# Optimization experiments

Hardware: AMD Instinct MI355X
Metric: run time of the kernel (lower is better)

## Reference

```python
import jax, jax.numpy as jnp
import numpy as np

N_NODES = 100000
N_EDGES = 1600000
IN_FEATS = 64
NUM_CLASSES = 64


def setup_inputs() -> dict:
    key = jax.random.key(0)
    k1, k2, k3, k4, k5, k6 = jax.random.split(key, 6)
    in_feat = jax.random.normal(k1, (N_NODES, IN_FEATS), dtype=jnp.float32)
    src = jax.random.randint(k2, (N_EDGES,), 0, N_NODES, dtype=jnp.int32)
    dst = jax.random.randint(k3, (N_EDGES,), 0, N_NODES, dtype=jnp.int32)
    scale = 1.0 / np.sqrt(IN_FEATS)
    W_self = jax.random.normal(k4, (IN_FEATS, NUM_CLASSES), dtype=jnp.float32) * scale
    W_neigh = jax.random.normal(k5, (IN_FEATS, NUM_CLASSES), dtype=jnp.float32) * scale
    bias = jax.random.normal(k6, (NUM_CLASSES,), dtype=jnp.float32) * 0.01
    return {"in_feat": in_feat, "src": src, "dst": dst,
            "W_self": W_self, "W_neigh": W_neigh, "bias": bias}


def reference(in_feat, src, dst, W_self, W_neigh, bias):
    # SAGEConv with 'mean' aggregator (DGL semantics):
    #   h_neigh[v] = mean over incoming edges (u->v) of in_feat[u]; 0 if no in-edges
    #   out = fc_self(x) + fc_neigh(h_neigh) + bias, then sigmoid
    n = in_feat.shape[0]
    msg = in_feat[src]                                            # [E, F] gather
    agg = jax.ops.segment_sum(msg, dst, num_segments=n)           # [N, F]
    deg = jax.ops.segment_sum(jnp.ones((src.shape[0],), jnp.float32), dst,
                              num_segments=n)                     # [N]
    h_neigh = agg / jnp.maximum(deg, 1.0)[:, None]                # mean, 0 for isolated
    out = in_feat @ W_self + h_neigh @ W_neigh + bias
    return jax.nn.sigmoid(out)
```

## Files before the change

### kernel.cpp

```cpp
#include <hip/hip_runtime.h>


constexpr int NN = 100000;
constexpr int NE = 1600000;
constexpr int F  = 64;
constexpr int RB = 256;
constexpr int NB = (NN + RB - 1) / RB;
constexpr int CH = 8192;
constexpr int PB = (NE + CH - 1) / CH;
constexpr int PREPB = (NN * F / 8 + 1024 + 255) / 256;
constexpr int SCAP = 3072;
constexpr int NP = 12;

typedef short bf16x8 __attribute__((ext_vector_type(8)));
typedef float f32x4  __attribute__((ext_vector_type(4)));
typedef float f32x2  __attribute__((ext_vector_type(2)));
typedef unsigned short u16;
typedef u16 u16x8 __attribute__((ext_vector_type(8)));

__device__ __forceinline__ u16 f2bf(float f) {
    unsigned u = __float_as_uint(f);
    unsigned r = (u + 0x7FFF + ((u >> 16) & 1)) >> 16;
    return (u16)r;
}

__device__ __forceinline__ void acc8pk(f32x2& a0, f32x2& a1, f32x2& a2, f32x2& a3,
                                       int2 qq) {
#if __has_builtin(__builtin_amdgcn_cvt_pk_f32_fp8)
    a0 += __builtin_amdgcn_cvt_pk_f32_fp8(qq.x, false);
    a1 += __builtin_amdgcn_cvt_pk_f32_fp8(qq.x, true);
    a2 += __builtin_amdgcn_cvt_pk_f32_fp8(qq.y, false);
    a3 += __builtin_amdgcn_cvt_pk_f32_fp8(qq.y, true);
#else
    a0[0] += __builtin_amdgcn_cvt_f32_fp8(qq.x, 0);
    a0[1] += __builtin_amdgcn_cvt_f32_fp8(qq.x, 1);
    a1[0] += __builtin_amdgcn_cvt_f32_fp8(qq.x, 2);
    a1[1] += __builtin_amdgcn_cvt_f32_fp8(qq.x, 3);
    a2[0] += __builtin_amdgcn_cvt_f32_fp8(qq.y, 0);
    a2[1] += __builtin_amdgcn_cvt_f32_fp8(qq.y, 1);
    a3[0] += __builtin_amdgcn_cvt_f32_fp8(qq.y, 2);
    a3[1] += __builtin_amdgcn_cvt_f32_fp8(qq.y, 3);
#endif
}

__global__ __launch_bounds__(256) void k_prep_hist(
    const float* __restrict__ x, const float* __restrict__ Ws,
    const float* __restrict__ Wn, const int* __restrict__ dst,
    unsigned char* __restrict__ x8, u16* __restrict__ xb, u16* __restrict__ Bt,
    int* __restrict__ gcount, int* __restrict__ donecnt,
    int* __restrict__ basep, int* __restrict__ cursor)
{
    const int bid = blockIdx.x;
    const int t   = threadIdx.x;

    if (bid < PREPB) {
        const int i = bid * 256 + t;
        if (i < NN * F / 8) {
            const int o = i * 8;
            float4 a = *(const float4*)&x[o];
            float4 b = *(const float4*)&x[o + 4];
            int lo = 0, hi = 0;
            lo = __builtin_amdgcn_cvt_pk_fp8_f32(a.x, a.y, lo, false);
            lo = __builtin_amdgcn_cvt_pk_fp8_f32(a.z, a.w, lo, true);
            hi = __builtin_amdgcn_cvt_pk_fp8_f32(b.x, b.y, hi, false);
            hi = __builtin_amdgcn_cvt_pk_fp8_f32(b.z, b.w, hi, true);
            *(int2*)&x8[o] = make_int2(lo, hi);
            u16x8 r;
            r[0] = f2bf(a.x); r[1] = f2bf(a.y); r[2] = f2bf(a.z); r[3] = f2bf(a.w);
            r[4] = f2bf(b.x); r[5] = f2bf(b.y); r[6] = f2bf(b.z); r[7] = f2bf(b.w);
            *(u16x8*)&xb[o] = r;
        } else if (i < NN * F / 8 + 1024) {
            const int j  = i - NN * F / 8;
            const int n  = j >> 4;
            const int kb = (j & 15) * 8;
            u16x8 r;
#pragma unroll
            for (int jj = 0; jj < 8; ++jj) {
                const int kk = kb + jj;
                const float w = (kk < 64) ? Ws[kk * 64 + n] : Wn[(kk - 64) * 64 + n];
                r[jj] = f2bf(w);
            }
            *(u16x8*)&Bt[n * 128 + kb] = r;
        }
        return;
    }

    __shared__ int h[NB];
    __shared__ int lastflag;
    for (int i = t; i < NB; i += 256) h[i] = 0;
    __syncthreads();
    const int hb  = bid - PREPB;
    const int b0  = hb * CH;
    const int end = min(b0 + CH, NE);
    for (int i = b0 + t * 4; i < end; i += 1024) {
        int4 d = *(const int4*)&dst[i];
        atomicAdd(&h[d.x >> 8], 1);
        atomicAdd(&h[d.y >> 8], 1);
        atomicAdd(&h[d.z >> 8], 1);
        atomicAdd(&h[d.w >> 8], 1);
    }
    __syncthreads();
    for (int i = t; i < NB; i += 256)
        if (h[i]) atomicAdd(&gcount[i], h[i]);

    __threadfence();
    if (t == 0) lastflag = (atomicAdd(donecnt, 1) == PB - 1);
    __syncthreads();
    if (!lastflag || t >= 64) return;

    int v[7], pre[7], s = 0;
#pragma unroll
    for (int j = 0; j < 7; ++j) {
        const int idx = t * 7 + j;
        v[j] = (idx < NB) ? atomicAdd(&gcount[idx], 0) : 0;
        pre[j] = s;
        s += v[j];
    }
    int run = s;
#pragma unroll
    for (int o = 1; o < 64; o <<= 1) {
        const int n = __shfl_up(run, o);
        if (t >= o) run += n;
    }
    const int lbase = run - s;
#pragma unroll
    for (int j = 0; j < 7; ++j) {
        const int idx = t * 7 + j;
        if (idx < NB) {
            basep[idx]  = lbase + pre[j];
            cursor[idx] = lbase + pre[j];
        }
    }
}

__global__ __launch_bounds__(512) void k_part(const int* __restrict__ src,
                                              const int* __restrict__ dst,
                                              int* __restrict__ cursor,
                                              unsigned* __restrict__ packed) {
    __shared__ unsigned stage[CH];
    __shared__ unsigned short bkt[CH];
    __shared__ int hist[NB], lscan[NB], lcur[NB], gpos[NB];
    __shared__ int tmp[512];

    const int t   = threadIdx.x;
    const int b0  = blockIdx.x * CH;
    const int cnt = min(CH, NE - b0);

    for (int i = t; i < NB; i += 512) hist[i] = 0;
    __syncthreads();

    int4 sv[4], dv[4];
#pragma unroll
    for (int j = 0; j < 4; ++j) {
        const int idx = j * 2048 + t * 4;
        if (idx < cnt) {
            sv[j] = *(const int4*)&src[b0 + idx];
            dv[j] = *(const int4*)&dst[b0 + idx];
            atomicAdd(&hist[dv[j].x >> 8], 1);
            atomicAdd(&hist[dv[j].y >> 8], 1);
            atomicAdd(&hist[dv[j].z >> 8], 1);
            atomicAdd(&hist[dv[j].w >> 8], 1);
        }
    }
    __syncthreads();

    int val = (t < NB) ? hist[t] : 0;
    tmp[t] = val;
    __syncthreads();
    int s = val;
    for (int o = 1; o < 512; o <<= 1) {
        int add = (t >= o) ? tmp[t - o] : 0;
        __syncthreads();
        s += add;
        tmp[t] = s;
        __syncthreads();
    }
    if (t < NB) {
        lscan[t] = s - val;
        lcur[t]  = s - val;
        gpos[t]  = val ? atomicAdd(&cursor[t], val) : 0;
    }
    __syncthreads();

#pragma unroll
    for (int j = 0; j < 4; ++j) {
        const int idx = j * 2048 + t * 4;
        if (idx < cnt) {
            const int ss[4] = {sv[j].x, sv[j].y, sv[j].z, sv[j].w};
            const int dd[4] = {dv[j].x, dv[j].y, dv[j].z, dv[j].w};
#pragma unroll
            for (int q = 0; q < 4; ++q) {
                const int b = dd[q] >> 8;
                const int p = atomicAdd(&lcur[b], 1);
                stage[p] = ((unsigned)(dd[q] & 255) << 17) | (unsigned)ss[q];
                bkt[p]   = (unsigned short)b;
            }
        }
    }
    __syncthreads();

    for (int i = t; i < cnt; i += 512) {
        const int b = bkt[i];
        packed[gpos[b] + (i - lscan[b])] = stage[i];
    }
}

__global__ __launch_bounds__(512) void k_fused(
    const unsigned char* __restrict__ x8, const u16* __restrict__ xb,
    const unsigned* __restrict__ packed, const int* __restrict__ basep,
    const u16* __restrict__ Bt, const float* __restrict__ bias,
    float* __restrict__ out)
{
    __shared__ u16 At[64 * 128];
    __shared__ unsigned stage[SCAP];
    __shared__ int hist[128], cur[128], exar[128];

    const int blk  = blockIdx.x;
    const int bu   = blk >> 1;
    const int hh   = blk & 1;
    const int base = bu * RB + hh * 128;
    const int t    = threadIdx.x;

    const int e0 = basep[bu];
    const int e1 = (bu == NB - 1) ? NE : basep[bu + 1];
    const int m  = e1 - e0;

    if (t < 128) hist[t] = 0;
    __syncthreads();

    unsigned pv[NP];
#pragma unroll
    for (int j = 0; j < NP; ++j) {
        const int i = t + j * 512;
        unsigned p = 0xFFFFFFFFu;
        if (i < m) p = packed[e0 + i];
        pv[j] = p;
        if (p != 0xFFFFFFFFu && ((p >> 24) & 1u) == (unsigned)hh)
            atomicAdd(&hist[(p >> 17) & 127], 1);
    }
    __syncthreads();

    if (t < 64) {
        const int v0 = hist[2 * t], v1 = hist[2 * t + 1];
        const int sv = v0 + v1;
        int run = sv;
#pragma unroll
        for (int o = 1; o < 64; o <<= 1) {
            const int n = __shfl_up(run, o);
            if (t >= o) run += n;
        }
        const int b0 = run - sv;
        exar[2 * t] = b0;      exar[2 * t + 1] = b0 + v0;
        cur[2 * t]  = b0;      cur[2 * t + 1]  = b0 + v0;
    }
    __syncthreads();

#pragma unroll
    for (int j = 0; j < NP; ++j) {
        const unsigned p = pv[j];
        if (p != 0xFFFFFFFFu && ((p >> 24) & 1u) == (unsigned)hh) {
            const int pos = atomicAdd(&cur[(p >> 17) & 127], 1);
            if (pos < SCAP) stage[pos] = p & 0x1FFFFu;
        }
    }
    __syncthreads();

    const int r    = t >> 3;
    const int cg   = t & 7;
    const int w    = t >> 6;
    const int lane = t & 63;
    const int tr   = w >> 1;
    const int nh   = w & 1;
    const int r16  = lane & 15;
    const int kg   = lane >> 4;

    for (int q = 0; q < 2; ++q) {
        const int nb64 = base + q * 64;
        const int nv_r = min(64, NN - nb64);

        if (nv_r > 0 && r < nv_r) {
            const int ln = q * 64 + r;
            const int dg = hist[ln];
            const int s0 = exar[ln];
            f32x2 a0 = {0.f, 0.f}, a1 = a0, a2 = a0, a3 = a0;
            int e = 0;
            for (; e + 4 <= dg; e += 4) {
                const int i0 = stage[s0 + e + 0];
                const int i1 = stage[s0 + e + 1];
                const int i2 = stage[s0 + e + 2];
                const int i3 = stage[s0 + e + 3];
                int2 q0 = *(const int2*)&x8[(size_t)i0 * F + cg * 8];
                int2 q1 = *(const int2*)&x8[(size_t)i1 * F + cg * 8];
                int2 q2 = *(const int2*)&x8[(size_t)i2 * F + cg * 8];
                int2 q3 = *(const int2*)&x8[(size_t)i3 * F + cg * 8];
                acc8pk(a0, a1, a2, a3, q0);
                acc8pk(a0, a1, a2, a3, q1);
                acc8pk(a0, a1, a2, a3, q2);
                acc8pk(a0, a1, a2, a3, q3);
            }
            for (; e < dg; ++e) {
                int2 qv = *(const int2*)&x8[(size_t)stage[s0 + e] * F + cg * 8];
                acc8pk(a0, a1, a2, a3, qv);
            }
            const float inv = 1.0f / fmaxf((float)dg, 1.0f);
            u16x8 hbv;
            hbv[0] = f2bf(a0[0] * inv); hbv[1] = f2bf(a0[1] * inv);
            hbv[2] = f2bf(a1[0] * inv); hbv[3] = f2bf(a1[1] * inv);
            hbv[4] = f2bf(a2[0] * inv); hbv[5] = f2bf(a2[1] * inv);
            hbv[6] = f2bf(a3[0] * inv); hbv[7] = f2bf(a3[1] * inv);
            const int bh = (8 + cg) ^ (r & 15);
            *(u16x8*)&At[r * 128 + bh * 8] = hbv;
            const int bx = cg ^ (r & 15);
            *(u16x8*)&At[r * 128 + bx * 8] = *(const u16x8*)&xb[(size_t)(nb64 + r) * F + cg * 8];
        }
        __syncthreads();

        if (nv_r > 0 && tr * 16 < nv_r) {
            bf16x8 bfr[4][2];
#pragma unroll
            for (int t4 = 0; t4 < 4; ++t4)
#pragma unroll
                for (int uu = 0; uu < 2; ++uu) {
                    const int n = (nh * 2 + uu) * 16 + r16;
                    bfr[t4][uu] = *(const bf16x8*)&Bt[n * 128 + t4 * 32 + kg * 8];
                }
            const float b0 = bias[(nh * 2 + 0) * 16 + r16];
            const float b1 = bias[(nh * 2 + 1) * 16 + r16];

            const int row = tr * 16 + r16;
            bf16x8 a[4];
#pragma unroll
            for (int t4 = 0; t4 < 4; ++t4) {
                const int blk16 = (t4 * 4 + kg) ^ (row & 15);
                a[t4] = *(const bf16x8*)&At[row * 128 + blk16 * 8];
            }

            f32x4 c0 = {0.f, 0.f, 0.f, 0.f}, c1 = c0;
            c0 = __builtin_amdgcn_mfma_f32_16x16x32_bf16(a[0], bfr[0][0], c0, 0, 0, 0);
            c0 = __builtin_amdgcn_mfma_f32_16x16x32_bf16(a[1], bfr[1][0], c0, 0, 0, 0);
            c0 = __builtin_amdgcn_mfma_f32_16x16x32_bf16(a[2], bfr[2][0], c0, 0, 0, 0);
            c0 = __builtin_amdgcn_mfma_f32_16x16x32_bf16(a[3], bfr[3][0], c0, 0, 0, 0);
            c1 = __builtin_amdgcn_mfma_f32_16x16x32_bf16(a[0], bfr[0][1], c1, 0, 0, 0);
            c1 = __builtin_amdgcn_mfma_f32_16x16x32_bf16(a[1], bfr[1][1], c1, 0, 0, 0);
            c1 = __builtin_amdgcn_mfma_f32_16x16x32_bf16(a[2], bfr[2][1], c1, 0, 0, 0);
            c1 = __builtin_amdgcn_mfma_f32_16x16x32_bf16(a[3], bfr[3][1], c1, 0, 0, 0);

            float* orow = out + (size_t)(nb64 + tr * 16) * 64;
#pragma unroll
            for (int rr = 0; rr < 4; ++rr) {
                const int ro = (kg * 4 + rr) * 64;
                orow[ro + (nh * 2 + 0) * 16 + r16] = 1.0f / (1.0f + __expf(-(c0[rr] + b0)));
                orow[ro + (nh * 2 + 1) * 16 + r16] = 1.0f / (1.0f + __expf(-(c1[rr] + b1)));
            }
        }
        __syncthreads();
    }
}

extern "C" void kernel_launch(void* const* d_in, const int* in_sizes, int n_in,
                              void* d_out, int out_size, void* d_ws, size_t ws_size,
                              hipStream_t stream) {
    const float* x    = (const float*)d_in[0];
    const int*   src  = (const int*)d_in[1];
    const int*   dst  = (const int*)d_in[2];
    const float* Ws   = (const float*)d_in[3];
    const float* Wn   = (const float*)d_in[4];
    const float* bias = (const float*)d_in[5];
    float* out = (float*)d_out;

    int* gcount  = (int*)d_ws;
    int* donecnt = gcount + NB;
    int* basep   = donecnt + 1;
    int* cursor  = basep + NB;
    unsigned* packed = (unsigned*)(cursor + NB);
    unsigned char* x8 = (unsigned char*)(packed + NE);
    u16* xb = (u16*)(x8 + (size_t)NN * F);
    u16* Bt = xb + (size_t)NN * F;

    hipMemsetAsync(gcount, 0, (size_t)(NB + 1) * sizeof(int), stream);

    k_prep_hist<<<PREPB + PB, 256, 0, stream>>>(x, Ws, Wn, dst, x8, xb, Bt,
                                                gcount, donecnt, basep, cursor);
    k_part <<<PB, 512, 0, stream>>>(src, dst, cursor, packed);
    k_fused<<<(NN + 127) / 128, 512, 0, stream>>>(x8, xb, packed, basep, Bt, bias, out);
}
```

Measured before the change: 102.8 us.

## Split fused SAGE blocks into quarters, drop bf16 x copy, sort edges by source half

The fused aggregation/GEMM kernel now runs four 64-node blocks per 256-node bucket instead of two 128-node blocks. Each block handles a single GEMM tile, with an overflow loop for edges beyond the register-held portion. The bf16 copy of x written in the prep kernel is removed, and the fused kernel converts fp32 x to bf16 on the fly. This trades a 12.8 MB write for a larger fp32 read. Edges are also keyed by a src-half bit so each node's neighbor list is grouped by source half for gather locality, and the partition chunk shrinks to 2048 so each thread handles one int4.

```diff
diff --git a/kernel.cpp b/kernel.cpp
--- a/kernel.cpp
+++ b/kernel.cpp
@@ -6,11 +6,12 @@
 constexpr int F  = 64;
 constexpr int RB = 256;
 constexpr int NB = (NN + RB - 1) / RB;
-constexpr int CH = 8192;
+constexpr int CH = 2048;
 constexpr int PB = (NE + CH - 1) / CH;
 constexpr int PREPB = (NN * F / 8 + 1024 + 255) / 256;
-constexpr int SCAP = 3072;
-constexpr int NP = 12;
+constexpr int HALF = 50000;
+constexpr int NP  = 9;
+constexpr int SCAP = 2048;
 
 typedef short bf16x8 __attribute__((ext_vector_type(8)));
 typedef float f32x4  __attribute__((ext_vector_type(4)));
@@ -46,7 +47,7 @@
 __global__ __launch_bounds__(256) void k_prep_hist(
     const float* __restrict__ x, const float* __restrict__ Ws,
     const float* __restrict__ Wn, const int* __restrict__ dst,
-    unsigned char* __restrict__ x8, u16* __restrict__ xb, u16* __restrict__ Bt,
+    unsigned char* __restrict__ x8, u16* __restrict__ Bt,
     int* __restrict__ gcount, int* __restrict__ donecnt,
     int* __restrict__ basep, int* __restrict__ cursor)
 {
@@ -65,10 +66,6 @@
             hi = __builtin_amdgcn_cvt_pk_fp8_f32(b.x, b.y, hi, false);
             hi = __builtin_amdgcn_cvt_pk_fp8_f32(b.z, b.w, hi, true);
             *(int2*)&x8[o] = make_int2(lo, hi);
-            u16x8 r;
-            r[0] = f2bf(a.x); r[1] = f2bf(a.y); r[2] = f2bf(a.z); r[3] = f2bf(a.w);
-            r[4] = f2bf(b.x); r[5] = f2bf(b.y); r[6] = f2bf(b.z); r[7] = f2bf(b.w);
-            *(u16x8*)&xb[o] = r;
         } else if (i < NN * F / 8 + 1024) {
             const int j  = i - NN * F / 8;
             const int n  = j >> 4;
@@ -149,18 +146,16 @@
     for (int i = t; i < NB; i += 512) hist[i] = 0;
     __syncthreads();
 
-    int4 sv[4], dv[4];
-#pragma unroll
-    for (int j = 0; j < 4; ++j) {
-        const int idx = j * 2048 + t * 4;
-        if (idx < cnt) {
-            sv[j] = *(const int4*)&src[b0 + idx];
-            dv[j] = *(const int4*)&dst[b0 + idx];
-            atomicAdd(&hist[dv[j].x >> 8], 1);
-            atomicAdd(&hist[dv[j].y >> 8], 1);
-            atomicAdd(&hist[dv[j].z >> 8], 1);
-            atomicAdd(&hist[dv[j].w >> 8], 1);
-        }
+    int4 sv, dv;
+    const int idx = t * 4;
+    const bool act = idx < cnt;
+    if (act) {
+        sv = *(const int4*)&src[b0 + idx];
+        dv = *(const int4*)&dst[b0 + idx];
+        atomicAdd(&hist[dv.x >> 8], 1);
+        atomicAdd(&hist[dv.y >> 8], 1);
+        atomicAdd(&hist[dv.z >> 8], 1);
+        atomicAdd(&hist[dv.w >> 8], 1);
     }
     __syncthreads();
 
@@ -182,19 +177,16 @@
     }
     __syncthreads();
 
-#pragma unroll
-    for (int j = 0; j < 4; ++j) {
-        const int idx = j * 2048 + t * 4;
-        if (idx < cnt) {
-            const int ss[4] = {sv[j].x, sv[j].y, sv[j].z, sv[j].w};
-            const int dd[4] = {dv[j].x, dv[j].y, dv[j].z, dv[j].w};
-#pragma unroll
-            for (int q = 0; q < 4; ++q) {
-                const int b = dd[q] >> 8;
-                const int p = atomicAdd(&lcur[b], 1);
-                stage[p] = ((unsigned)(dd[q] & 255) << 17) | (unsigned)ss[q];
-                bkt[p]   = (unsigned short)b;
-            }
+    if (act) {
+        const int ss[4] = {sv.x, sv.y, sv.z, sv.w};
+        const int dd[4] = {dv.x, dv.y, dv.z, dv.w};
+#pragma unroll
+        for (int q = 0; q < 4; ++q) {
+            const int b = dd[q] >> 8;
+            const int p = atomicAdd(&lcur[b], 1);
+            stage[p] = ((unsigned)(dd[q] & 255) << 18) |
+                       ((unsigned)(ss[q] >= HALF) << 17) | (unsigned)ss[q];
+            bkt[p]   = (unsigned short)b;
         }
     }
     __syncthreads();
@@ -206,7 +198,7 @@
 }
 
 __global__ __launch_bounds__(512) void k_fused(
-    const unsigned char* __restrict__ x8, const u16* __restrict__ xb,
+    const unsigned char* __restrict__ x8, const float* __restrict__ x,
     const unsigned* __restrict__ packed, const int* __restrict__ basep,
     const u16* __restrict__ Bt, const float* __restrict__ bias,
     float* __restrict__ out)
@@ -216,10 +208,11 @@
     __shared__ int hist[128], cur[128], exar[128];
 
     const int blk  = blockIdx.x;
-    const int bu   = blk >> 1;
-    const int hh   = blk & 1;
-    const int base = bu * RB + hh * 128;
+    const int bu   = blk >> 2;
+    const int qq   = blk & 3;
+    const int base = bu * RB + qq * 64;
     const int t    = threadIdx.x;
+    const int nv   = min(64, NN - base);
 
     const int e0 = basep[bu];
     const int e1 = (bu == NB - 1) ? NE : basep[bu + 1];
@@ -235,8 +228,12 @@
         unsigned p = 0xFFFFFFFFu;
         if (i < m) p = packed[e0 + i];
         pv[j] = p;
-        if (p != 0xFFFFFFFFu && ((p >> 24) & 1u) == (unsigned)hh)
+        if (p != 0xFFFFFFFFu && (int)((p >> 24) & 3) == qq)
             atomicAdd(&hist[(p >> 17) & 127], 1);
+    }
+    for (int i = NP * 512 + t; i < m; i += 512) {
+        const unsigned p = packed[e0 + i];
+        if ((int)((p >> 24) & 3) == qq) atomicAdd(&hist[(p >> 17) & 127], 1);
     }
     __syncthreads();
 
@@ -258,102 +255,107 @@
 #pragma unroll
     for (int j = 0; j < NP; ++j) {
         const unsigned p = pv[j];
-        if (p != 0xFFFFFFFFu && ((p >> 24) & 1u) == (unsigned)hh) {
+        if (p != 0xFFFFFFFFu && (int)((p >> 24) & 3) == qq) {
             const int pos = atomicAdd(&cur[(p >> 17) & 127], 1);
             if (pos < SCAP) stage[pos] = p & 0x1FFFFu;
         }
     }
-    __syncthreads();
-
-    const int r    = t >> 3;
-    const int cg   = t & 7;
+    for (int i = NP * 512 + t; i < m; i += 512) {
+        const unsigned p = packed[e0 + i];
+        if ((int)((p >> 24) & 3) == qq) {
+            const int pos = atomicAdd(&cur[(p >> 17) & 127], 1);
+            if (pos < SCAP) stage[pos] = p & 0x1FFFFu;
+        }
+    }
+    __syncthreads();
+
+    const int r  = t >> 3;
+    const int cg = t & 7;
+    if (r < nv) {
+        const int dg = hist[2 * r] + hist[2 * r + 1];
+        const int s0 = exar[2 * r];
+        f32x2 a0 = {0.f, 0.f}, a1 = a0, a2 = a0, a3 = a0;
+        int e = 0;
+        for (; e + 4 <= dg; e += 4) {
+            const int i0 = stage[s0 + e + 0];
+            const int i1 = stage[s0 + e + 1];
+            const int i2 = stage[s0 + e + 2];
+            const int i3 = stage[s0 + e + 3];
+            int2 q0 = *(const int2*)&x8[(size_t)i0 * F + cg * 8];
+            int2 q1 = *(const int2*)&x8[(size_t)i1 * F + cg * 8];
+            int2 q2 = *(const int2*)&x8[(size_t)i2 * F + cg * 8];
+            int2 q3 = *(const int2*)&x8[(size_t)i3 * F + cg * 8];
+            acc8pk(a0, a1, a2, a3, q0);
+            acc8pk(a0, a1, a2, a3, q1);
+            acc8pk(a0, a1, a2, a3, q2);
+            acc8pk(a0, a1, a2, a3, q3);
+        }
+        for (; e < dg; ++e) {
+            int2 qv = *(const int2*)&x8[(size_t)stage[s0 + e] * F + cg * 8];
+            acc8pk(a0, a1, a2, a3, qv);
+        }
+        const float inv = 1.0f / fmaxf((float)dg, 1.0f);
+        u16x8 hbv;
+        hbv[0] = f2bf(a0[0] * inv); hbv[1] = f2bf(a0[1] * inv);
+        hbv[2] = f2bf(a1[0] * inv); hbv[3] = f2bf(a1[1] * inv);
+        hbv[4] = f2bf(a2[0] * inv); hbv[5] = f2bf(a2[1] * inv);
+        hbv[6] = f2bf(a3[0] * inv); hbv[7] = f2bf(a3[1] * inv);
+        const int bh = (8 + cg) ^ (r & 15);
+        *(u16x8*)&At[r * 128 + bh * 8] = hbv;
+
+        float4 xa = *(const float4*)&x[(size_t)(base + r) * F + cg * 8];
+        float4 xc = *(const float4*)&x[(size_t)(base + r) * F + cg * 8 + 4];
+        u16x8 xv;
+        xv[0] = f2bf(xa.x); xv[1] = f2bf(xa.y); xv[2] = f2bf(xa.z); xv[3] = f2bf(xa.w);
+        xv[4] = f2bf(xc.x); xv[5] = f2bf(xc.y); xv[6] = f2bf(xc.z); xv[7] = f2bf(xc.w);
+        const int bx = cg ^ (r & 15);
+        *(u16x8*)&At[r * 128 + bx * 8] = xv;
+    }
+    __syncthreads();
+
     const int w    = t >> 6;
     const int lane = t & 63;
     const int tr   = w >> 1;
-    const int nh   = w & 1;
-    const int r16  = lane & 15;
-    const int kg   = lane >> 4;
-
-    for (int q = 0; q < 2; ++q) {
-        const int nb64 = base + q * 64;
-        const int nv_r = min(64, NN - nb64);
-
-        if (nv_r > 0 && r < nv_r) {
-            const int ln = q * 64 + r;
-            const int dg = hist[ln];
-            const int s0 = exar[ln];
-            f32x2 a0 = {0.f, 0.f}, a1 = a0, a2 = a0, a3 = a0;
-            int e = 0;
-            for (; e + 4 <= dg; e += 4) {
-                const int i0 = stage[s0 + e + 0];
-                const int i1 = stage[s0 + e + 1];
-                const int i2 = stage[s0 + e + 2];
-                const int i3 = stage[s0 + e + 3];
-                int2 q0 = *(const int2*)&x8[(size_t)i0 * F + cg * 8];
-                int2 q1 = *(const int2*)&x8[(size_t)i1 * F + cg * 8];
-                int2 q2 = *(const int2*)&x8[(size_t)i2 * F + cg * 8];
-                int2 q3 = *(const int2*)&x8[(size_t)i3 * F + cg * 8];
-                acc8pk(a0, a1, a2, a3, q0);
-                acc8pk(a0, a1, a2, a3, q1);
-                acc8pk(a0, a1, a2, a3, q2);
-                acc8pk(a0, a1, a2, a3, q3);
-            }
-            for (; e < dg; ++e) {
-                int2 qv = *(const int2*)&x8[(size_t)stage[s0 + e] * F + cg * 8];
-                acc8pk(a0, a1, a2, a3, qv);
-            }
-            const float inv = 1.0f / fmaxf((float)dg, 1.0f);
-            u16x8 hbv;
-            hbv[0] = f2bf(a0[0] * inv); hbv[1] = f2bf(a0[1] * inv);
-            hbv[2] = f2bf(a1[0] * inv); hbv[3] = f2bf(a1[1] * inv);
-            hbv[4] = f2bf(a2[0] * inv); hbv[5] = f2bf(a2[1] * inv);
-            hbv[6] = f2bf(a3[0] * inv); hbv[7] = f2bf(a3[1] * inv);
-            const int bh = (8 + cg) ^ (r & 15);
-            *(u16x8*)&At[r * 128 + bh * 8] = hbv;
-            const int bx = cg ^ (r & 15);
-            *(u16x8*)&At[r * 128 + bx * 8] = *(const u16x8*)&xb[(size_t)(nb64 + r) * F + cg * 8];
-        }
-        __syncthreads();
-
-        if (nv_r > 0 && tr * 16 < nv_r) {
-            bf16x8 bfr[4][2];
-#pragma unroll
-            for (int t4 = 0; t4 < 4; ++t4)
-#pragma unroll
-                for (int uu = 0; uu < 2; ++uu) {
-                    const int n = (nh * 2 + uu) * 16 + r16;
-                    bfr[t4][uu] = *(const bf16x8*)&Bt[n * 128 + t4 * 32 + kg * 8];
-                }
-            const float b0 = bias[(nh * 2 + 0) * 16 + r16];
-            const float b1 = bias[(nh * 2 + 1) * 16 + r16];
-
-            const int row = tr * 16 + r16;
-            bf16x8 a[4];
-#pragma unroll
-            for (int t4 = 0; t4 < 4; ++t4) {
-                const int blk16 = (t4 * 4 + kg) ^ (row & 15);
-                a[t4] = *(const bf16x8*)&At[row * 128 + blk16 * 8];
-            }
-
-            f32x4 c0 = {0.f, 0.f, 0.f, 0.f}, c1 = c0;
-            c0 = __builtin_amdgcn_mfma_f32_16x16x32_bf16(a[0], bfr[0][0], c0, 0, 0, 0);
-            c0 = __builtin_amdgcn_mfma_f32_16x16x32_bf16(a[1], bfr[1][0], c0, 0, 0, 0);
-            c0 = __builtin_amdgcn_mfma_f32_16x16x32_bf16(a[2], bfr[2][0], c0, 0, 0, 0);
-            c0 = __builtin_amdgcn_mfma_f32_16x16x32_bf16(a[3], bfr[3][0], c0, 0, 0, 0);
-            c1 = __builtin_amdgcn_mfma_f32_16x16x32_bf16(a[0], bfr[0][1], c1, 0, 0, 0);
-            c1 = __builtin_amdgcn_mfma_f32_16x16x32_bf16(a[1], bfr[1][1], c1, 0, 0, 0);
-            c1 = __builtin_amdgcn_mfma_f32_16x16x32_bf16(a[2], bfr[2][1], c1, 0, 0, 0);
-            c1 = __builtin_amdgcn_mfma_f32_16x16x32_bf16(a[3], bfr[3][1], c1, 0, 0, 0);
-
-            float* orow = out + (size_t)(nb64 + tr * 16) * 64;
-#pragma unroll
-            for (int rr = 0; rr < 4; ++rr) {
-                const int ro = (kg * 4 + rr) * 64;
-                orow[ro + (nh * 2 + 0) * 16 + r16] = 1.0f / (1.0f + __expf(-(c0[rr] + b0)));
-                orow[ro + (nh * 2 + 1) * 16 + r16] = 1.0f / (1.0f + __expf(-(c1[rr] + b1)));
-            }
-        }
-        __syncthreads();
+    if (tr * 16 >= nv) return;
+    const int nh  = w & 1;
+    const int r16 = lane & 15;
+    const int kg  = lane >> 4;
+
+    bf16x8 bfr[4][2];
+#pragma unroll
+    for (int t4 = 0; t4 < 4; ++t4)
+#pragma unroll
+        for (int uu = 0; uu < 2; ++uu) {
+            const int n = (nh * 2 + uu) * 16 + r16;
+            bfr[t4][uu] = *(const bf16x8*)&Bt[n * 128 + t4 * 32 + kg * 8];
+        }
+    const float b0 = bias[(nh * 2 + 0) * 16 + r16];
+    const float b1 = bias[(nh * 2 + 1) * 16 + r16];
+
+    const int row = tr * 16 + r16;
+    bf16x8 a[4];
+#pragma unroll
+    for (int t4 = 0; t4 < 4; ++t4) {
+        const int blk16 = (t4 * 4 + kg) ^ (row & 15);
+        a[t4] = *(const bf16x8*)&At[row * 128 + blk16 * 8];
+    }
+
+    f32x4 c0 = {0.f, 0.f, 0.f, 0.f}, c1 = c0;
+    c0 = __builtin_amdgcn_mfma_f32_16x16x32_bf16(a[0], bfr[0][0], c0, 0, 0, 0);
+    c0 = __builtin_amdgcn_mfma_f32_16x16x32_bf16(a[1], bfr[1][0], c0, 0, 0, 0);
+    c0 = __builtin_amdgcn_mfma_f32_16x16x32_bf16(a[2], bfr[2][0], c0, 0, 0, 0);
+    c0 = __builtin_amdgcn_mfma_f32_16x16x32_bf16(a[3], bfr[3][0], c0, 0, 0, 0);
+    c1 = __builtin_amdgcn_mfma_f32_16x16x32_bf16(a[0], bfr[0][1], c1, 0, 0, 0);
+    c1 = __builtin_amdgcn_mfma_f32_16x16x32_bf16(a[1], bfr[1][1], c1, 0, 0, 0);
+    c1 = __builtin_amdgcn_mfma_f32_16x16x32_bf16(a[2], bfr[2][1], c1, 0, 0, 0);
+    c1 = __builtin_amdgcn_mfma_f32_16x16x32_bf16(a[3], bfr[3][1], c1, 0, 0, 0);
+
+    float* orow = out + (size_t)(base + tr * 16) * 64;
+#pragma unroll
+    for (int rr = 0; rr < 4; ++rr) {
+        const int ro = (kg * 4 + rr) * 64;
+        orow[ro + (nh * 2 + 0) * 16 + r16] = 1.0f / (1.0f + __expf(-(c0[rr] + b0)));
+        orow[ro + (nh * 2 + 1) * 16 + r16] = 1.0f / (1.0f + __expf(-(c1[rr] + b1)));
     }
 }
 
@@ -374,13 +376,12 @@
     int* cursor  = basep + NB;
     unsigned* packed = (unsigned*)(cursor + NB);
     unsigned char* x8 = (unsigned char*)(packed + NE);
-    u16* xb = (u16*)(x8 + (size_t)NN * F);
-    u16* Bt = xb + (size_t)NN * F;
+    u16* Bt = (u16*)(x8 + (size_t)NN * F);
 
     hipMemsetAsync(gcount, 0, (size_t)(NB + 1) * sizeof(int), stream);
 
-    k_prep_hist<<<PREPB + PB, 256, 0, stream>>>(x, Ws, Wn, dst, x8, xb, Bt,
+    k_prep_hist<<<PREPB + PB, 256, 0, stream>>>(x, Ws, Wn, dst, x8, Bt,
                                                 gcount, donecnt, basep, cursor);
     k_part <<<PB, 512, 0, stream>>>(src, dst, cursor, packed);
-    k_fused<<<(NN + 127) / 128, 512, 0, stream>>>(x8, xb, packed, basep, Bt, bias, out);
-}
+    k_fused<<<NB * 4, 512, 0, stream>>>(x8, x, packed, basep, Bt, bias, out);
+}
```

Result: slower. 142.9 us (+39.0%).

## Process full 256-node buckets per block with source-quartile sub-sorting and nontemporal stores

Applied to the files above, without the earlier changes.

The fused kernel now handles a whole 256-destination bucket per block (391 blocks) instead of splitting each bucket across two blocks that both read the full packed edge list. Edges are also sub-sorted by source quartile (a new 2-bit field in the packed word), which is meant to improve gather locality in the fp8 feature table. Nontemporal loads and stores are added for the packed, xb and output streams. In exchange there are fewer blocks, hence less parallelism, a 512-step block-wide scan with many syncs, a larger shared stage buffer that may lower occupancy, and a SCAP overflow risk if a bucket has more than 5120 edges.

```diff
diff --git a/kernel.cpp b/kernel.cpp
--- a/kernel.cpp
+++ b/kernel.cpp
@@ -9,14 +9,16 @@
 constexpr int CH = 8192;
 constexpr int PB = (NE + CH - 1) / CH;
 constexpr int PREPB = (NN * F / 8 + 1024 + 255) / 256;
-constexpr int SCAP = 3072;
-constexpr int NP = 12;
+constexpr int QSZ = 25000;
+constexpr int NP  = 10;
+constexpr int SCAP = 5120;
 
 typedef short bf16x8 __attribute__((ext_vector_type(8)));
 typedef float f32x4  __attribute__((ext_vector_type(4)));
 typedef float f32x2  __attribute__((ext_vector_type(2)));
 typedef unsigned short u16;
 typedef u16 u16x8 __attribute__((ext_vector_type(8)));
+typedef unsigned u32x4 __attribute__((ext_vector_type(4)));
 
 __device__ __forceinline__ u16 f2bf(float f) {
     unsigned u = __float_as_uint(f);
@@ -68,7 +70,7 @@
             u16x8 r;
             r[0] = f2bf(a.x); r[1] = f2bf(a.y); r[2] = f2bf(a.z); r[3] = f2bf(a.w);
             r[4] = f2bf(b.x); r[5] = f2bf(b.y); r[6] = f2bf(b.z); r[7] = f2bf(b.w);
-            *(u16x8*)&xb[o] = r;
+            __builtin_nontemporal_store(*(u32x4*)&r, (u32x4*)&xb[o]);
         } else if (i < NN * F / 8 + 1024) {
             const int j  = i - NN * F / 8;
             const int n  = j >> 4;
@@ -190,9 +192,11 @@
             const int dd[4] = {dv[j].x, dv[j].y, dv[j].z, dv[j].w};
 #pragma unroll
             for (int q = 0; q < 4; ++q) {
-                const int b = dd[q] >> 8;
-                const int p = atomicAdd(&lcur[b], 1);
-                stage[p] = ((unsigned)(dd[q] & 255) << 17) | (unsigned)ss[q];
+                const int b   = dd[q] >> 8;
+                const int qtr = ss[q] / QSZ;
+                const int p   = atomicAdd(&lcur[b], 1);
+                stage[p] = ((unsigned)(dd[q] & 255) << 19) |
+                           ((unsigned)qtr << 17) | (unsigned)ss[q];
                 bkt[p]   = (unsigned short)b;
             }
         }
@@ -201,7 +205,7 @@
 
     for (int i = t; i < cnt; i += 512) {
         const int b = bkt[i];
-        packed[gpos[b] + (i - lscan[b])] = stage[i];
+        __builtin_nontemporal_store(stage[i], &packed[gpos[b] + (i - lscan[b])]);
     }
 }
 
@@ -212,20 +216,22 @@
     float* __restrict__ out)
 {
     __shared__ u16 At[64 * 128];
-    __shared__ unsigned stage[SCAP];
-    __shared__ int hist[128], cur[128], exar[128];
-
-    const int blk  = blockIdx.x;
-    const int bu   = blk >> 1;
-    const int hh   = blk & 1;
-    const int base = bu * RB + hh * 128;
+    __shared__ int stage[SCAP];
+    __shared__ int hist[1024];
+    __shared__ int ex[1024];
+    __shared__ int cur[1024];
+    __shared__ int tmp[512];
+
+    const int b    = blockIdx.x;
+    const int base = b * RB;
     const int t    = threadIdx.x;
-
-    const int e0 = basep[bu];
-    const int e1 = (bu == NB - 1) ? NE : basep[bu + 1];
+    const int nv   = min(RB, NN - base);
+
+    const int e0 = basep[b];
+    const int e1 = (b == NB - 1) ? NE : basep[b + 1];
     const int m  = e1 - e0;
 
-    if (t < 128) hist[t] = 0;
+    hist[t] = 0; hist[t + 512] = 0;
     __syncthreads();
 
     unsigned pv[NP];
@@ -233,35 +239,47 @@
     for (int j = 0; j < NP; ++j) {
         const int i = t + j * 512;
         unsigned p = 0xFFFFFFFFu;
-        if (i < m) p = packed[e0 + i];
+        if (i < m) p = __builtin_nontemporal_load(&packed[e0 + i]);
         pv[j] = p;
-        if (p != 0xFFFFFFFFu && ((p >> 24) & 1u) == (unsigned)hh)
-            atomicAdd(&hist[(p >> 17) & 127], 1);
-    }
-    __syncthreads();
-
-    if (t < 64) {
-        const int v0 = hist[2 * t], v1 = hist[2 * t + 1];
-        const int sv = v0 + v1;
-        int run = sv;
-#pragma unroll
-        for (int o = 1; o < 64; o <<= 1) {
-            const int n = __shfl_up(run, o);
-            if (t >= o) run += n;
-        }
-        const int b0 = run - sv;
-        exar[2 * t] = b0;      exar[2 * t + 1] = b0 + v0;
-        cur[2 * t]  = b0;      cur[2 * t + 1]  = b0 + v0;
-    }
+        if (p != 0xFFFFFFFFu) atomicAdd(&hist[(p >> 17) & 1023], 1);
+    }
+    for (int i = NP * 512 + t; i < m; i += 512) {
+        const unsigned p = __builtin_nontemporal_load(&packed[e0 + i]);
+        atomicAdd(&hist[(p >> 17) & 1023], 1);
+    }
+    __syncthreads();
+
+    const int v0 = hist[2 * t], v1 = hist[2 * t + 1];
+    const int sv = v0 + v1;
+    tmp[t] = sv;
+    __syncthreads();
+    int s = sv;
+    for (int o = 1; o < 512; o <<= 1) {
+        int add = (t >= o) ? tmp[t - o] : 0;
+        __syncthreads();
+        s += add;
+        tmp[t] = s;
+        __syncthreads();
+    }
+    const int excl = s - sv;
+    ex[2 * t]     = excl;
+    ex[2 * t + 1] = excl + v0;
+    cur[2 * t]     = excl;
+    cur[2 * t + 1] = excl + v0;
     __syncthreads();
 
 #pragma unroll
     for (int j = 0; j < NP; ++j) {
         const unsigned p = pv[j];
-        if (p != 0xFFFFFFFFu && ((p >> 24) & 1u) == (unsigned)hh) {
-            const int pos = atomicAdd(&cur[(p >> 17) & 127], 1);
-            if (pos < SCAP) stage[pos] = p & 0x1FFFFu;
-        }
+        if (p != 0xFFFFFFFFu) {
+            const int pos = atomicAdd(&cur[(p >> 17) & 1023], 1);
+            if (pos < SCAP) stage[pos] = (int)(p & 0x1FFFFu);
+        }
+    }
+    for (int i = NP * 512 + t; i < m; i += 512) {
+        const unsigned p = __builtin_nontemporal_load(&packed[e0 + i]);
+        const int pos = atomicAdd(&cur[(p >> 17) & 1023], 1);
+        if (pos < SCAP) stage[pos] = (int)(p & 0x1FFFFu);
     }
     __syncthreads();
 
@@ -274,14 +292,15 @@
     const int r16  = lane & 15;
     const int kg   = lane >> 4;
 
-    for (int q = 0; q < 2; ++q) {
-        const int nb64 = base + q * 64;
-        const int nv_r = min(64, NN - nb64);
-
-        if (nv_r > 0 && r < nv_r) {
-            const int ln = q * 64 + r;
-            const int dg = hist[ln];
-            const int s0 = exar[ln];
+    for (int gq = 0; gq * 64 < nv; ++gq) {
+        const int nb64 = base + gq * 64;
+        const int nvr  = min(64, nv - gq * 64);
+
+        if (r < nvr) {
+            const int ln = gq * 64 + r;
+            const int s0 = ex[4 * ln];
+            const int dg = hist[4 * ln] + hist[4 * ln + 1] +
+                           hist[4 * ln + 2] + hist[4 * ln + 3];
             f32x2 a0 = {0.f, 0.f}, a1 = a0, a2 = a0, a3 = a0;
             int e = 0;
             for (; e + 4 <= dg; e += 4) {
@@ -310,12 +329,14 @@
             hbv[6] = f2bf(a3[0] * inv); hbv[7] = f2bf(a3[1] * inv);
             const int bh = (8 + cg) ^ (r & 15);
             *(u16x8*)&At[r * 128 + bh * 8] = hbv;
-            const int bx = cg ^ (r & 15);
-            *(u16x8*)&At[r * 128 + bx * 8] = *(const u16x8*)&xb[(size_t)(nb64 + r) * F + cg * 8];
-        }
-        __syncthreads();
-
-        if (nv_r > 0 && tr * 16 < nv_r) {
+
+            u32x4 xw = __builtin_nontemporal_load(
+                (const u32x4*)&xb[(size_t)(nb64 + r) * F + cg * 8]);
+            *(u32x4*)&At[r * 128 + (cg ^ (r & 15)) * 8] = xw;
+        }
+        __syncthreads();
+
+        if (tr * 16 < nvr) {
             bf16x8 bfr[4][2];
 #pragma unroll
             for (int t4 = 0; t4 < 4; ++t4)
@@ -324,8 +345,8 @@
                     const int n = (nh * 2 + uu) * 16 + r16;
                     bfr[t4][uu] = *(const bf16x8*)&Bt[n * 128 + t4 * 32 + kg * 8];
                 }
-            const float b0 = bias[(nh * 2 + 0) * 16 + r16];
-            const float b1 = bias[(nh * 2 + 1) * 16 + r16];
+            const float b0v = bias[(nh * 2 + 0) * 16 + r16];
+            const float b1v = bias[(nh * 2 + 1) * 16 + r16];
 
             const int row = tr * 16 + r16;
             bf16x8 a[4];
@@ -349,8 +370,10 @@
 #pragma unroll
             for (int rr = 0; rr < 4; ++rr) {
                 const int ro = (kg * 4 + rr) * 64;
-                orow[ro + (nh * 2 + 0) * 16 + r16] = 1.0f / (1.0f + __expf(-(c0[rr] + b0)));
-                orow[ro + (nh * 2 + 1) * 16 + r16] = 1.0f / (1.0f + __expf(-(c1[rr] + b1)));
+                __builtin_nontemporal_store(1.0f / (1.0f + __expf(-(c0[rr] + b0v))),
+                                            &orow[ro + (nh * 2 + 0) * 16 + r16]);
+                __builtin_nontemporal_store(1.0f / (1.0f + __expf(-(c1[rr] + b1v))),
+                                            &orow[ro + (nh * 2 + 1) * 16 + r16]);
             }
         }
         __syncthreads();
@@ -377,10 +400,10 @@
     u16* xb = (u16*)(x8 + (size_t)NN * F);
     u16* Bt = xb + (size_t)NN * F;
 
-    hipMemsetAsync(gcount, 0, (size_t)(NB + 1) * sizeof(int), stream);
+    (void)hipMemsetAsync(gcount, 0, (size_t)(NB + 1) * sizeof(int), stream);
 
     k_prep_hist<<<PREPB + PB, 256, 0, stream>>>(x, Ws, Wn, dst, x8, xb, Bt,
                                                 gcount, donecnt, basep, cursor);
     k_part <<<PB, 512, 0, stream>>>(src, dst, cursor, packed);
-    k_fused<<<(NN + 127) / 128, 512, 0, stream>>>(x8, xb, packed, basep, Bt, bias, out);
-}
+    k_fused<<<NB, 512, 0, stream>>>(x8, xb, packed, basep, Bt, bias, out);
+}
```

Result: faster. 98.94 us (-3.7%).
